# Performance work log

Measured on AMD Instinct MI355X. Metric: run time of the kernel, lower is better.

Reference implementation:

```python
import jax, jax.numpy as jnp
import numpy as np

H, HD, RD = 16, 128, 64          # n_heads, head_dim, rope_dim
CD = HD - RD                      # content_dim = 64
THETA = 10000.0


def apply_rope(x, cos, sin):
    # x: [B,H,T,RD]; cos/sin: [T,RD//2] broadcast over B,H
    d = x.shape[-1] // 2
    x1, x2 = x[..., :d], x[..., d:]
    return jnp.concatenate([x1 * cos - x2 * sin, x1 * sin + x2 * cos], axis=-1)


def setup_inputs() -> dict:
    key = jax.random.key(0)
    ks = jax.random.split(key, 9)
    d_model, q_rank, d_latent = 2048, 512, 512
    B, T = 2, 2048
    s = 0.02
    return {
        "x": jax.random.normal(ks[0], (B, T, d_model), dtype=jnp.float32),
        "Wq_down": jax.random.normal(ks[1], (d_model, q_rank), dtype=jnp.float32) * s,
        "Wq_up": jax.random.normal(ks[2], (q_rank, H * CD), dtype=jnp.float32) * s,
        "Wq_rope": jax.random.normal(ks[3], (d_model, H * RD), dtype=jnp.float32) * s,
        "Wkv_down": jax.random.normal(ks[4], (d_model, d_latent), dtype=jnp.float32) * s,
        "Wk_up": jax.random.normal(ks[5], (d_latent, H * CD), dtype=jnp.float32) * s,
        "Wv_up": jax.random.normal(ks[6], (d_latent, H * HD), dtype=jnp.float32) * s,
        "Wk_rope": jax.random.normal(ks[7], (d_model, H * RD), dtype=jnp.float32) * s,
        "Wo": jax.random.normal(ks[8], (H * HD, d_model), dtype=jnp.float32) * s,
    }


def reference(x, Wq_down, Wq_up, Wq_rope, Wkv_down, Wk_up, Wv_up, Wk_rope, Wo):
    B, T, _ = x.shape

    # low-rank projections
    q_content = (x @ Wq_down) @ Wq_up            # [B,T,H*CD]
    q_pos = x @ Wq_rope                          # [B,T,H*RD]
    kv_latent = x @ Wkv_down                     # [B,T,d_latent]
    k_content = kv_latent @ Wk_up                # [B,T,H*CD]
    k_pos = x @ Wk_rope                          # [B,T,H*RD]
    v = kv_latent @ Wv_up                        # [B,T,H*HD]

    def split_heads(t, d):
        return t.reshape(B, T, H, d).transpose(0, 2, 1, 3)  # [B,H,T,d]

    q_content = split_heads(q_content, CD)
    q_pos = split_heads(q_pos, RD)
    k_content = split_heads(k_content, CD)
    k_pos = split_heads(k_pos, RD)
    v = split_heads(v, HD)

    # rotary tables: [T, RD//2]
    inv_freq = 1.0 / (THETA ** (jnp.arange(0, RD, 2, dtype=jnp.float32) / RD))
    freqs = jnp.arange(T, dtype=jnp.float32)[:, None] * inv_freq[None, :]
    cos, sin = jnp.cos(freqs), jnp.sin(freqs)

    q_pos = apply_rope(q_pos, cos, sin)
    k_pos = apply_rope(k_pos, cos, sin)

    q = jnp.concatenate([q_content, q_pos], axis=-1)  # [B,H,T,HD]
    k = jnp.concatenate([k_content, k_pos], axis=-1)  # [B,H,T,HD]

    # causal SDPA, scale = 1/sqrt(head_dim)
    scale = 1.0 / jnp.sqrt(jnp.asarray(HD, dtype=q.dtype))
    scores = jnp.einsum("bhqd,bhkd->bhqk", q, k) * scale
    causal = jnp.tril(jnp.ones((T, T), dtype=bool))
    scores = jnp.where(causal, scores, jnp.finfo(scores.dtype).min)
    attn = jax.nn.softmax(scores, axis=-1)
    out = jnp.einsum("bhqk,bhkd->bhqd", attn, v)      # [B,H,T,HD]

    out = out.transpose(0, 2, 1, 3).reshape(B, T, H * HD)
    return out @ Wo
```

## Files before the change

### kernel.cpp

```cpp
#include <hip/hip_runtime.h>
#include <hip/hip_bf16.h>
#include <stdint.h>
#include <math.h>

#define H_ 16
#define HD_ 128
#define RD_ 64
#define CD_ 64
#define DM_ 2048
#define QR_ 512
#define DL_ 512
#define B_ 2
#define T_ 2048
#define M_TOT (B_*T_)

typedef __attribute__((ext_vector_type(8))) short short8;
typedef __attribute__((ext_vector_type(4))) float f32x4;
typedef __attribute__((ext_vector_type(16))) float f32x16;

__device__ __forceinline__ unsigned short f2b_hw(float f){
  __hip_bfloat16 h = __float2bfloat16(f);
  union { __hip_bfloat16 h; unsigned short u; } c; c.h = h; return c.u;
}
__device__ __forceinline__ float b2f(unsigned short b){
  union { unsigned u; float f; } a; a.u = ((unsigned)b) << 16;
  return a.f;
}
__device__ __forceinline__ unsigned pack2(float lo, float hi){
  __hip_bfloat162 h2 = __float22bfloat162_rn(make_float2(lo, hi));
  union { __hip_bfloat162 h; unsigned u; } c; c.h = h2; return c.u;
}

#define GLOAD16(g, l) __builtin_amdgcn_global_load_lds( \
    (__attribute__((address_space(1))) void*)(g), \
    (__attribute__((address_space(3))) void*)(l), 16, 0, 0)

__global__ void cast_f32_bf16(const float* __restrict__ src,
                              unsigned short* __restrict__ dst, int n){
  int i = (blockIdx.x * blockDim.x + threadIdx.x) * 4;
  if (i < n){
    float4 v = *(const float4*)(src + i);
    ushort4 o;
    o.x = f2b_hw(v.x); o.y = f2b_hw(v.y); o.z = f2b_hw(v.z); o.w = f2b_hw(v.w);
    *(ushort4*)(dst + i) = o;
  }
}

__global__ void rope_table(float2* __restrict__ tab){
  int idx = blockIdx.x * 256 + threadIdx.x;
  int t = idx >> 5, j = idx & 31;
  float invf = exp2f(-(float)j * 0.4152410118750f);
  float fr = (float)t * invf;
  float s, c;
  sincosf(fr, &s, &c);
  tab[idx] = make_float2(c, s);
}

struct TTe { const float* src; unsigned short* dst; int K, N, blk0; };
struct TT8 { TTe e[8]; };

__global__ void transpose_cast8(TT8 tab){
  __shared__ float tile[32][33];
  int bid = blockIdx.x;
  const float* src = tab.e[0].src;
  unsigned short* dst = tab.e[0].dst;
  int K = tab.e[0].K, N = tab.e[0].N, loc = bid;
  #pragma unroll
  for (int j = 1; j < 8; j++){
    if (bid >= tab.e[j].blk0){
      src = tab.e[j].src; dst = tab.e[j].dst;
      K = tab.e[j].K; N = tab.e[j].N; loc = bid - tab.e[j].blk0;
    }
  }
  int cols = N / 32;
  int n0 = (loc % cols) * 32, k0 = (loc / cols) * 32;
  int tx = threadIdx.x, ty = threadIdx.y;
  #pragma unroll
  for (int r = ty; r < 32; r += 8)
    tile[r][tx] = src[(size_t)(k0 + r) * N + n0 + tx];
  __syncthreads();
  #pragma unroll
  for (int r = ty; r < 32; r += 8)
    dst[(size_t)(n0 + r) * K + k0 + tx] = f2b_hw(tile[tx][r]);
}

template<int MODE>
__global__ __launch_bounds__(512, 1) void gemm256(
    const unsigned short* __restrict__ A, int lda,
    const unsigned short* __restrict__ Bt,
    void* __restrict__ Cv, void* __restrict__ Cv2, void* __restrict__ Cv3,
    const float2* __restrict__ tab,
    int ldc, int N, int K)
{
  __shared__ __align__(16) unsigned short lds[65536];
  char* ldsb = (char*)lds;

  const int tid = threadIdx.x;
  const int lane = tid & 63, w = tid >> 6;
  const int wm = w >> 2, wn = w & 3;
  const int l15 = lane & 15, kg = lane >> 4;

  int gx = gridDim.x;
  int nwg = gx * gridDim.y;
  int lin = blockIdx.x + gx * blockIdx.y;
  int q8 = nwg >> 3;
  int nl = (lin & 7) * q8 + (lin >> 3);
  int m0 = (nl / gx) * 256, n0 = (nl % gx) * 256;

  const unsigned short* Aeff = A;
  if (MODE == 5 && n0 >= 1024) Aeff = A + 512;

  const int srow = tid >> 3;
  const int scol = ((((tid & 7) << 4) ^ (((tid >> 5) & 1) << 5)) >> 1);
  const int aswz = ((l15 >> 2) & 1) << 5;

#define STG(bufb, kt) do {                                                     \
    int k0_ = (kt) * 64;                                                       \
    _Pragma("unroll")                                                          \
    for (int h_ = 0; h_ < 2; h_++)                                             \
      _Pragma("unroll")                                                        \
      for (int i_ = 0; i_ < 2; i_++) {                                         \
        GLOAD16(Aeff + (size_t)(m0 + h_*128 + i_*64 + srow) * lda + k0_ + scol,\
                ldsb + (bufb)*65536 + h_*16384 + i_*8192 + tid*16);            \
        GLOAD16(Bt + (size_t)(n0 + h_*128 + i_*64 + srow) * K + k0_ + scol,    \
                ldsb + (bufb)*65536 + 32768 + h_*16384 + i_*8192 + tid*16);    \
      }                                                                        \
  } while (0)

  f32x4 acc[8][4];
  #pragma unroll
  for (int i = 0; i < 8; i++)
    #pragma unroll
    for (int j = 0; j < 4; j++)
      acc[i][j] = (f32x4){0.f, 0.f, 0.f, 0.f};

  const int nK = K >> 6;
  STG(0, 0);
  STG(1, 1);

  for (int t = 0; t < nK; t++) {
    const int c = t & 1;
    if (t < nK - 1) { asm volatile("s_waitcnt vmcnt(8)" ::: "memory"); }
    else            { asm volatile("s_waitcnt vmcnt(0)" ::: "memory"); }
    __builtin_amdgcn_s_barrier();
    __builtin_amdgcn_sched_barrier(0);

    const char* bufA = ldsb + c * 65536 + wm * 16384;
    const char* bufB = ldsb + c * 65536 + 32768;

    short8 bfr[4][2];
    #pragma unroll
    for (int nf = 0; nf < 4; nf++) {
      int nr = wn * 64 + nf * 16 + l15;
      #pragma unroll
      for (int kk = 0; kk < 2; kk++) {
        int L = (nr & 127) * 128 + kk * 64 + kg * 16;
        bfr[nf][kk] = *(const short8*)(bufB + (nr >> 7) * 16384 + (L ^ aswz));
      }
    }
    __builtin_amdgcn_s_setprio(1);
    #pragma unroll
    for (int mh = 0; mh < 2; mh++) {
      short8 afr[4][2];
      #pragma unroll
      for (int q = 0; q < 4; q++) {
        int mf = mh * 4 + q;
        #pragma unroll
        for (int kk = 0; kk < 2; kk++) {
          int L = (mf * 16 + l15) * 128 + kk * 64 + kg * 16;
          afr[q][kk] = *(const short8*)(bufA + (L ^ aswz));
        }
      }
      #pragma unroll
      for (int q = 0; q < 4; q++)
        #pragma unroll
        for (int nf = 0; nf < 4; nf++)
          #pragma unroll
          for (int kk = 0; kk < 2; kk++)
            acc[mh*4+q][nf] = __builtin_amdgcn_mfma_f32_16x16x32_bf16(
                afr[q][kk], bfr[nf][kk], acc[mh*4+q][nf], 0, 0, 0);
    }
    __builtin_amdgcn_s_setprio(0);
    __builtin_amdgcn_sched_barrier(0);
    __builtin_amdgcn_s_barrier();
    __builtin_amdgcn_sched_barrier(0);
    if (t + 2 < nK) STG(c, t + 2);
  }
#undef STG

  if (MODE == 4) {
    if (n0 < 1024) {
      unsigned short* C = (unsigned short*)Cv;
      #pragma unroll
      for (int mf = 0; mf < 8; mf++)
        #pragma unroll
        for (int nf = 0; nf < 4; nf++)
          #pragma unroll
          for (int rr = 0; rr < 4; rr++) {
            int row = m0 + wm * 128 + mf * 16 + kg * 4 + rr;
            int col = n0 + wn * 64 + nf * 16 + l15;
            C[(size_t)row * ldc + col] = f2b_hw(acc[mf][nf][rr]);
          }
    } else {
      const bool isq = (n0 < 2048);
      unsigned short* dst = (unsigned short*)(isq ? Cv2 : Cv3);
      int hbase = ((n0 - (isq ? 1024 : 2048)) >> 6) + wn;
      #pragma unroll
      for (int nf = 0; nf < 2; nf++) {
        int jr = nf * 16 + l15;
        #pragma unroll
        for (int mf = 0; mf < 8; mf++)
          #pragma unroll
          for (int rr = 0; rr < 4; rr++) {
            int gr = m0 + wm * 128 + mf * 16 + kg * 4 + rr;
            int tt = gr & (T_ - 1), bb = gr >> 11;
            float2 cs = tab[tt * 32 + jr];
            float x1 = acc[mf][nf][rr], x2 = acc[mf][nf + 2][rr];
            size_t base = ((size_t)(bb * H_ + hbase) * T_ + tt) * 128 + 64;
            dst[base + jr]      = f2b_hw(x1 * cs.x - x2 * cs.y);
            dst[base + jr + 32] = f2b_hw(x1 * cs.y + x2 * cs.x);
          }
      }
    }
  } else {
    if (n0 < 2048) {
      unsigned short* dstp = (unsigned short*)(n0 < 1024 ? Cv : Cv2);
      int cb0 = n0 - (n0 < 1024 ? 0 : 1024);
      #pragma unroll
      for (int nf = 0; nf < 4; nf++) {
        int colb = cb0 + wn * 64 + nf * 16 + l15;
        int h = colb >> 6, d = colb & 63;
        #pragma unroll
        for (int mf = 0; mf < 8; mf++)
          #pragma unroll
          for (int rr = 0; rr < 4; rr++) {
            int gr = m0 + wm * 128 + mf * 16 + kg * 4 + rr;
            size_t idx = ((size_t)((gr >> 11) * H_ + h) * T_ + (gr & (T_-1))) * 128 + d;
            dstp[idx] = f2b_hw(acc[mf][nf][rr]);
          }
      }
    } else {
      unsigned short* vtp = (unsigned short*)Cv3;
      #pragma unroll
      for (int nf = 0; nf < 4; nf++) {
        int c2 = n0 + wn * 64 + nf * 16 + l15 - 2048;
        int h = c2 >> 7, d = c2 & 127;
        #pragma unroll
        for (int mf = 0; mf < 8; mf++) {
          int gr0 = m0 + wm * 128 + mf * 16 + kg * 4;
          int bb = gr0 >> 11, t0 = gr0 & (T_-1);
          ushort4 o;
          o.x = f2b_hw(acc[mf][nf][0]); o.y = f2b_hw(acc[mf][nf][1]);
          o.z = f2b_hw(acc[mf][nf][2]); o.w = f2b_hw(acc[mf][nf][3]);
          *(ushort4*)&vtp[((size_t)(bb * H_ + h) * 128 + d) * T_ + t0] = o;
        }
      }
    }
  }
}

__global__ __launch_bounds__(512, 1) void gemm_out(
    const unsigned short* __restrict__ A, int lda,
    const unsigned short* __restrict__ Bt,
    float* __restrict__ C, int ldc, int K)
{
  __shared__ __align__(16) unsigned short lds[49152];
  char* ldsb = (char*)lds;

  const int tid = threadIdx.x;
  const int lane = tid & 63, w = tid >> 6;
  const int wm = w >> 2, wn = w & 3;
  const int l15 = lane & 15, kg = lane >> 4;

  int gx = gridDim.x;
  int nwg = gx * gridDim.y;
  int lin = blockIdx.x + gx * blockIdx.y;
  int q8 = nwg >> 3;
  int nl = (lin & 7) * q8 + (lin >> 3);
  int m0 = (nl / gx) * 128, n0 = (nl % gx) * 256;

  const int srow = tid >> 3;
  const int scol = ((((tid & 7) << 4) ^ (((tid >> 5) & 1) << 5)) >> 1);
  const int aswz = ((l15 >> 2) & 1) << 5;

#define STG(bufb, kt) do {                                                     \
    int k0_ = (kt) * 64;                                                       \
    _Pragma("unroll")                                                          \
    for (int i_ = 0; i_ < 2; i_++)                                             \
      GLOAD16(A + (size_t)(m0 + i_*64 + srow) * lda + k0_ + scol,              \
              ldsb + (bufb)*49152 + i_*8192 + tid*16);                         \
    _Pragma("unroll")                                                          \
    for (int i_ = 0; i_ < 4; i_++)                                             \
      GLOAD16(Bt + (size_t)(n0 + i_*64 + srow) * K + k0_ + scol,               \
              ldsb + (bufb)*49152 + 16384 + i_*8192 + tid*16);                 \
  } while (0)

  f32x4 acc[4][4];
  #pragma unroll
  for (int i = 0; i < 4; i++)
    #pragma unroll
    for (int j = 0; j < 4; j++)
      acc[i][j] = (f32x4){0.f, 0.f, 0.f, 0.f};

  const int nK = K >> 6;
  STG(0, 0);
  STG(1, 1);

  for (int t = 0; t < nK; t++) {
    const int c = t & 1;
    if (t < nK - 1) { asm volatile("s_waitcnt vmcnt(6)" ::: "memory"); }
    else            { asm volatile("s_waitcnt vmcnt(0)" ::: "memory"); }
    __builtin_amdgcn_s_barrier();
    __builtin_amdgcn_sched_barrier(0);

    const char* bufA = ldsb + c * 49152 + wm * 8192;
    const char* bufB = ldsb + c * 49152 + 16384;

    short8 bfr[4][2];
    #pragma unroll
    for (int nf = 0; nf < 4; nf++) {
      int nr = wn * 64 + nf * 16 + l15;
      #pragma unroll
      for (int kk = 0; kk < 2; kk++) {
        int L = (nr & 63) * 128 + kk * 64 + kg * 16;
        bfr[nf][kk] = *(const short8*)(bufB + (nr >> 6) * 8192 + (L ^ aswz));
      }
    }
    short8 afr[4][2];
    #pragma unroll
    for (int mf = 0; mf < 4; mf++)
      #pragma unroll
      for (int kk = 0; kk < 2; kk++) {
        int L = (mf * 16 + l15) * 128 + kk * 64 + kg * 16;
        afr[mf][kk] = *(const short8*)(bufA + (L ^ aswz));
      }
    __builtin_amdgcn_s_setprio(1);
    #pragma unroll
    for (int mf = 0; mf < 4; mf++)
      #pragma unroll
      for (int nf = 0; nf < 4; nf++)
        #pragma unroll
        for (int kk = 0; kk < 2; kk++)
          acc[mf][nf] = __builtin_amdgcn_mfma_f32_16x16x32_bf16(
              afr[mf][kk], bfr[nf][kk], acc[mf][nf], 0, 0, 0);
    __builtin_amdgcn_s_setprio(0);
    __builtin_amdgcn_sched_barrier(0);
    __builtin_amdgcn_s_barrier();
    __builtin_amdgcn_sched_barrier(0);
    if (t + 2 < nK) STG(c, t + 2);
  }
#undef STG

  #pragma unroll
  for (int mf = 0; mf < 4; mf++)
    #pragma unroll
    for (int nf = 0; nf < 4; nf++)
      #pragma unroll
      for (int rr = 0; rr < 4; rr++) {
        int row = m0 + wm * 64 + mf * 16 + kg * 4 + rr;
        int col = n0 + wn * 64 + nf * 16 + l15;
        C[(size_t)row * ldc + col] = acc[mf][nf][rr];
      }
}

__global__ __launch_bounds__(256, 2) void attn_fwd7(
    const unsigned short* __restrict__ qh,
    const unsigned short* __restrict__ kh,
    const unsigned short* __restrict__ vt,
    unsigned short* __restrict__ ao)
{
  __shared__ __align__(16) unsigned short lds[4 * 8192];

  const int tid  = threadIdx.x;
  const int lane = tid & 63, w = tid >> 6;
  const int l31  = lane & 31, hi = lane >> 5;
  const int bh = blockIdx.y;
  const int b  = bh >> 4, hd = bh & 15;
  int qt = blockIdx.x;
  if (bh >= 16) qt = 15 - qt;
  const int q0w   = qt * 128 + w * 32;
  const int qg    = q0w + l31;
  const int qmaxw = q0w + 31;
  const int nt    = 2 * qt + 2;

  const unsigned short* Qg = qh + (size_t)bh * T_ * 128;
  const unsigned short* Kg = kh + (size_t)bh * T_ * 128;
  const unsigned short* Vg = vt + (size_t)bh * 128 * T_;

  short8 qf[8];
  #pragma unroll
  for (int kc = 0; kc < 8; kc++)
    qf[kc] = *(const short8*)&Qg[(size_t)qg * 128 + kc * 16 + hi * 8];

  f32x16 accO[4];
  #pragma unroll
  for (int sb = 0; sb < 4; sb++)
    #pragma unroll
    for (int r = 0; r < 16; r++) accO[sb][r] = 0.f;

  float m = -1e30f, lsum = 0.f;
  const float SC = 0.12751743f;

  int krow[4], kwof[4], vrow[4], vwof[4];
  #pragma unroll
  for (int jj = 0; jj < 4; jj++){
    int r_ = (w * 4 + jj) * 4 + (lane >> 4);
    krow[jj] = r_;
    kwof[jj] = r_ * 128 + ((((lane & 15) * 16) ^ ((r_ & 7) << 4)) >> 1);
    int d_ = (w * 4 + jj) * 8 + (lane >> 3);
    vrow[jj] = d_;
    vwof[jj] = d_ * 64 + ((((lane & 7) * 16) ^ ((d_ & 7) << 4)) >> 1);
  }
  const int kcol = (lane & 15) * 8;
  const int vcol = (lane & 7) * 8;

  uint4 kst[4], vst[4];

#define REG_LOAD(kvt) do {                                                    \
    int kv0s = (kvt) * 64;                                                    \
    _Pragma("unroll")                                                         \
    for (int j_ = 0; j_ < 4; j_++) {                                          \
      kst[j_] = *(const uint4*)&Kg[(size_t)(kv0s + krow[j_]) * 128 + kcol];   \
      vst[j_] = *(const uint4*)&Vg[(size_t)vrow[j_] * T_ + kv0s + vcol];      \
    }                                                                         \
  } while (0)

#define DS_WRITE(bufi) do {                                                   \
    unsigned short* ksb_ = lds + (bufi) * 8192;                               \
    unsigned short* vsb_ = lds + 16384 + (bufi) * 8192;                       \
    _Pragma("unroll")                                                         \
    for (int j_ = 0; j_ < 4; j_++) {                                          \
      *(uint4*)&ksb_[kwof[j_]] = kst[j_];                                     \
      *(uint4*)&vsb_[vwof[j_]] = vst[j_];                                     \
    }                                                                         \
  } while (0)

  REG_LOAD(0);
  DS_WRITE(0);
  if (nt > 1) REG_LOAD(1);
  asm volatile("s_waitcnt lgkmcnt(0)" ::: "memory");
  __builtin_amdgcn_s_barrier();
  __builtin_amdgcn_sched_barrier(0);

  for (int t = 0; t < nt; t++) {
    const int cur = t & 1;
    if (t + 1 < nt) DS_WRITE(cur ^ 1);
    if (t + 2 < nt) REG_LOAD(t + 2);
    const int kv0 = t * 64;
    if (kv0 <= qmaxw) {
      const unsigned short* Kb = lds + cur * 8192;
      const unsigned short* Vb = lds + 16384 + cur * 8192;

      f32x16 sa0, sa1;
      #pragma unroll
      for (int r = 0; r < 16; r++) { sa0[r] = 0.f; sa1[r] = 0.f; }
      __builtin_amdgcn_s_setprio(1);
      #pragma unroll
      for (int kc = 0; kc < 8; kc++) {
        int co = (kc * 32 + hi * 16);
        int r0 = l31;
        short8 kf0 = *(const short8*)&Kb[r0 * 128 + ((co ^ ((r0 & 7) << 4)) >> 1)];
        sa0 = __builtin_amdgcn_mfma_f32_32x32x16_bf16(kf0, qf[kc], sa0, 0, 0, 0);
        int r1 = 32 + l31;
        short8 kf1 = *(const short8*)&Kb[r1 * 128 + ((co ^ ((r1 & 7) << 4)) >> 1)];
        sa1 = __builtin_amdgcn_mfma_f32_32x32x16_bf16(kf1, qf[kc], sa1, 0, 0, 0);
      }
      __builtin_amdgcn_s_setprio(0);

      float p0[16], p1[16];
      float pmax = -1e30f;
      bool needMask = (kv0 + 63 > q0w);
      if (needMask) {
        #pragma unroll
        for (int r = 0; r < 16; r++) {
          int crow = (r & 3) + 8 * (r >> 2) + 4 * hi;
          float v0 = sa0[r] * SC;
          float v1 = sa1[r] * SC;
          if (kv0 + crow > qg)      v0 = -1e30f;
          if (kv0 + 32 + crow > qg) v1 = -1e30f;
          p0[r] = v0; p1[r] = v1;
          pmax = fmaxf(pmax, fmaxf(v0, v1));
        }
      } else {
        #pragma unroll
        for (int r = 0; r < 16; r++) {
          float v0 = sa0[r] * SC;
          float v1 = sa1[r] * SC;
          p0[r] = v0; p1[r] = v1;
          pmax = fmaxf(pmax, fmaxf(v0, v1));
        }
      }
      pmax = fmaxf(pmax, __shfl_xor(pmax, 32, 64));
      if (!__all(pmax <= m + 8.f)) {
        float mn  = fmaxf(m, pmax);
        float fac = exp2f(m - mn);
        m = mn;
        lsum *= fac;
        #pragma unroll
        for (int sb = 0; sb < 4; sb++)
          #pragma unroll
          for (int r = 0; r < 16; r++) accO[sb][r] *= fac;
      }
      float ls = 0.f;
      #pragma unroll
      for (int r = 0; r < 16; r++) {
        p0[r] = exp2f(p0[r] - m);
        p1[r] = exp2f(p1[r] - m);
        ls += p0[r] + p1[r];
      }
      ls += __shfl_xor(ls, 32, 64);
      lsum += ls;

      #pragma unroll
      for (int kc2 = 0; kc2 < 4; kc2++) {
        unsigned A01, A23, B01, B23;
        if (kc2 == 0) { A01 = pack2(p0[0], p0[1]);  A23 = pack2(p0[2], p0[3]);
                        B01 = pack2(p0[4], p0[5]);  B23 = pack2(p0[6], p0[7]); }
        else if (kc2 == 1) { A01 = pack2(p0[8], p0[9]);   A23 = pack2(p0[10], p0[11]);
                             B01 = pack2(p0[12], p0[13]); B23 = pack2(p0[14], p0[15]); }
        else if (kc2 == 2) { A01 = pack2(p1[0], p1[1]);  A23 = pack2(p1[2], p1[3]);
                             B01 = pack2(p1[4], p1[5]);  B23 = pack2(p1[6], p1[7]); }
        else { A01 = pack2(p1[8], p1[9]);   A23 = pack2(p1[10], p1[11]);
               B01 = pack2(p1[12], p1[13]); B23 = pack2(p1[14], p1[15]); }
        asm("v_permlane32_swap_b32 %0, %1" : "+v"(A01), "+v"(B01));
        asm("v_permlane32_swap_b32 %0, %1" : "+v"(A23), "+v"(B23));
        union { unsigned u[4]; short8 v; } pk;
        pk.u[0] = A01; pk.u[1] = A23; pk.u[2] = B01; pk.u[3] = B23;
        short8 pa = pk.v;
        __builtin_amdgcn_s_setprio(1);
        #pragma unroll
        for (int sb = 0; sb < 4; sb++) {
          int d = sb * 32 + l31;
          short8 vf = *(const short8*)&Vb[d * 64 + (((kc2 * 32 + hi * 16) ^ ((d & 7) << 4)) >> 1)];
          accO[sb] = __builtin_amdgcn_mfma_f32_32x32x16_bf16(vf, pa, accO[sb], 0, 0, 0);
        }
        __builtin_amdgcn_s_setprio(0);
      }
    }
    __builtin_amdgcn_sched_barrier(0);
    asm volatile("s_waitcnt lgkmcnt(0)" ::: "memory");
    __builtin_amdgcn_s_barrier();
    __builtin_amdgcn_sched_barrier(0);
  }

  float rl = 1.0f / lsum;
  size_t orow = ((size_t)b * T_ + qg) * (H_*HD_) + hd * 128;
  #pragma unroll
  for (int sb = 0; sb < 4; sb++)
    #pragma unroll
    for (int g = 0; g < 4; g++) {
      ushort4 o;
      o.x = f2b_hw(accO[sb][4 * g + 0] * rl);
      o.y = f2b_hw(accO[sb][4 * g + 1] * rl);
      o.z = f2b_hw(accO[sb][4 * g + 2] * rl);
      o.w = f2b_hw(accO[sb][4 * g + 3] * rl);
      *(ushort4*)&ao[orow + sb * 32 + 8 * g + 4 * hi] = o;
    }
#undef REG_LOAD
#undef DS_WRITE
}

extern "C" void kernel_launch(void* const* d_in, const int* in_sizes, int n_in,
                              void* d_out, int out_size, void* d_ws, size_t ws_size,
                              hipStream_t stream)
{
  (void)in_sizes; (void)n_in; (void)out_size; (void)ws_size;
  const float* x        = (const float*)d_in[0];
  const float* Wq_down  = (const float*)d_in[1];
  const float* Wq_up    = (const float*)d_in[2];
  const float* Wq_rope  = (const float*)d_in[3];
  const float* Wkv_down = (const float*)d_in[4];
  const float* Wk_up    = (const float*)d_in[5];
  const float* Wv_up    = (const float*)d_in[6];
  const float* Wk_rope  = (const float*)d_in[7];
  const float* Wo       = (const float*)d_in[8];

  char* ws = (char*)d_ws;
  unsigned short* xb      = (unsigned short*)(ws + 0);
  unsigned short* Wdall   = (unsigned short*)(ws + 16777216);
  unsigned short* WquT    = (unsigned short*)(ws + 29360128);
  unsigned short* WkcvT   = (unsigned short*)(ws + 30408704);
  unsigned short* WoT     = (unsigned short*)(ws + 33554432);
  unsigned short* projall = (unsigned short*)(ws + 41943040);
  unsigned short* qh      = (unsigned short*)(ws + 67108864);
  unsigned short* kh      = (unsigned short*)(ws + 83886080);
  unsigned short* vt      = (unsigned short*)(ws + 100663296);
  unsigned short* ao      = (unsigned short*)(ws + 117440512);
  float2*         ctab    = (float2*)(ws + 134217728);

  dim3 tb(32, 8);

  cast_f32_bf16<<<(M_TOT * DM_ / 4 + 255) / 256, 256, 0, stream>>>(x, xb, M_TOT * DM_);
  rope_table<<<256, 256, 0, stream>>>(ctab);

  TT8 tab;
  int blk = 0;
  tab.e[0] = { Wq_down,  Wdall,               DM_, QR_,     blk }; blk += (QR_/32)*(DM_/32);
  tab.e[1] = { Wkv_down, Wdall + 512*2048,    DM_, DL_,     blk }; blk += (DL_/32)*(DM_/32);
  tab.e[2] = { Wq_rope,  Wdall + 1024*2048,   DM_, H_*RD_,  blk }; blk += (H_*RD_/32)*(DM_/32);
  tab.e[3] = { Wk_rope,  Wdall + 2048*2048,   DM_, H_*RD_,  blk }; blk += (H_*RD_/32)*(DM_/32);
  tab.e[4] = { Wq_up,    WquT,                QR_, H_*CD_,  blk }; blk += (H_*CD_/32)*(QR_/32);
  tab.e[5] = { Wk_up,    WkcvT,               DL_, H_*CD_,  blk }; blk += (H_*CD_/32)*(DL_/32);
  tab.e[6] = { Wv_up,    WkcvT + 1024*512,    DL_, H_*HD_,  blk }; blk += (H_*HD_/32)*(DL_/32);
  tab.e[7] = { Wo,       WoT,                 H_*HD_, DM_,  blk }; blk += (DM_/32)*(H_*HD_/32);
  transpose_cast8<<<blk, tb, 0, stream>>>(tab);

  gemm256<4><<<dim3(3072/256, M_TOT/256), 512, 0, stream>>>(
      xb, DM_, Wdall, projall, qh, kh, ctab, 1024, 3072, DM_);
  gemm256<5><<<dim3(4096/256, M_TOT/256), 512, 0, stream>>>(
      projall, 1024, WquT, qh, kh, vt, nullptr, 0, 4096, DL_);

  attn_fwd7<<<dim3(16, 32), 256, 0, stream>>>(qh, kh, vt, ao);

  gemm_out<<<dim3(DM_/256, M_TOT/128), 512, 0, stream>>>(
      ao, 2048, WoT, (float*)d_out, DM_, H_*HD_);
}
```

Measured before the change: 301.4 us.

## Merge rope table into cast kernel, vectorize weight transpose, split QK accumulators

Folds the rope cos/sin table generation into the x cast kernel as extra blocks, which saves one kernel launch. The weight transpose-cast now uses float4 loads and ushort4 stores with an 8x32 thread block. In the attention kernel, the QK^T MFMA chain is split into two independent accumulator pairs that are summed at the end. This shortens MFMA dependency chains at the cost of more accumulator registers, which may put pressure on occupancy. The LDS pattern in the transpose changes and may introduce bank conflicts.

```diff
diff --git a/kernel.cpp b/kernel.cpp
--- a/kernel.cpp
+++ b/kernel.cpp
@@ -36,24 +36,26 @@
     (__attribute__((address_space(3))) void*)(l), 16, 0, 0)
 
 __global__ void cast_f32_bf16(const float* __restrict__ src,
-                              unsigned short* __restrict__ dst, int n){
-  int i = (blockIdx.x * blockDim.x + threadIdx.x) * 4;
+                              unsigned short* __restrict__ dst, int n,
+                              float2* __restrict__ tab){
+  int bid = blockIdx.x;
+  if (bid >= 8192) {
+    int idx = (bid - 8192) * 256 + threadIdx.x;
+    int t = idx >> 5, j = idx & 31;
+    float invf = exp2f(-(float)j * 0.4152410118750f);
+    float fr = (float)t * invf;
+    float s, c;
+    sincosf(fr, &s, &c);
+    tab[idx] = make_float2(c, s);
+    return;
+  }
+  int i = (bid * 256 + threadIdx.x) * 4;
   if (i < n){
     float4 v = *(const float4*)(src + i);
     ushort4 o;
     o.x = f2b_hw(v.x); o.y = f2b_hw(v.y); o.z = f2b_hw(v.z); o.w = f2b_hw(v.w);
     *(ushort4*)(dst + i) = o;
   }
-}
-
-__global__ void rope_table(float2* __restrict__ tab){
-  int idx = blockIdx.x * 256 + threadIdx.x;
-  int t = idx >> 5, j = idx & 31;
-  float invf = exp2f(-(float)j * 0.4152410118750f);
-  float fr = (float)t * invf;
-  float s, c;
-  sincosf(fr, &s, &c);
-  tab[idx] = make_float2(c, s);
 }
 
 struct TTe { const float* src; unsigned short* dst; int K, N, blk0; };
@@ -75,13 +77,18 @@
   int cols = N / 32;
   int n0 = (loc % cols) * 32, k0 = (loc / cols) * 32;
   int tx = threadIdx.x, ty = threadIdx.y;
-  #pragma unroll
-  for (int r = ty; r < 32; r += 8)
-    tile[r][tx] = src[(size_t)(k0 + r) * N + n0 + tx];
+  float4 v = *(const float4*)&src[(size_t)(k0 + ty) * N + n0 + tx * 4];
+  tile[ty][tx * 4 + 0] = v.x;
+  tile[ty][tx * 4 + 1] = v.y;
+  tile[ty][tx * 4 + 2] = v.z;
+  tile[ty][tx * 4 + 3] = v.w;
   __syncthreads();
-  #pragma unroll
-  for (int r = ty; r < 32; r += 8)
-    dst[(size_t)(n0 + r) * K + k0 + tx] = f2b_hw(tile[tx][r]);
+  ushort4 o;
+  o.x = f2b_hw(tile[tx * 4 + 0][ty]);
+  o.y = f2b_hw(tile[tx * 4 + 1][ty]);
+  o.z = f2b_hw(tile[tx * 4 + 2][ty]);
+  o.w = f2b_hw(tile[tx * 4 + 3][ty]);
+  *(ushort4*)&dst[(size_t)(n0 + ty) * K + k0 + tx * 4] = o;
 }
 
 template<int MODE>
@@ -363,7 +370,7 @@
       }
 }
 
-__global__ __launch_bounds__(256, 2) void attn_fwd7(
+__global__ __launch_bounds__(256, 2) void attn_fwd8(
     const unsigned short* __restrict__ qh,
     const unsigned short* __restrict__ kh,
     const unsigned short* __restrict__ vt,
@@ -451,21 +458,27 @@
       const unsigned short* Kb = lds + cur * 8192;
       const unsigned short* Vb = lds + 16384 + cur * 8192;
 
-      f32x16 sa0, sa1;
-      #pragma unroll
-      for (int r = 0; r < 16; r++) { sa0[r] = 0.f; sa1[r] = 0.f; }
+      f32x16 sa0, sa1, sb0, sb1;
+      #pragma unroll
+      for (int r = 0; r < 16; r++) { sa0[r] = 0.f; sa1[r] = 0.f; sb0[r] = 0.f; sb1[r] = 0.f; }
       __builtin_amdgcn_s_setprio(1);
       #pragma unroll
-      for (int kc = 0; kc < 8; kc++) {
-        int co = (kc * 32 + hi * 16);
-        int r0 = l31;
-        short8 kf0 = *(const short8*)&Kb[r0 * 128 + ((co ^ ((r0 & 7) << 4)) >> 1)];
-        sa0 = __builtin_amdgcn_mfma_f32_32x32x16_bf16(kf0, qf[kc], sa0, 0, 0, 0);
-        int r1 = 32 + l31;
-        short8 kf1 = *(const short8*)&Kb[r1 * 128 + ((co ^ ((r1 & 7) << 4)) >> 1)];
-        sa1 = __builtin_amdgcn_mfma_f32_32x32x16_bf16(kf1, qf[kc], sa1, 0, 0, 0);
+      for (int kc = 0; kc < 8; kc += 2) {
+        int co0 = (kc * 32 + hi * 16);
+        int co1 = ((kc + 1) * 32 + hi * 16);
+        int r0 = l31, r1 = 32 + l31;
+        short8 kf0a = *(const short8*)&Kb[r0 * 128 + ((co0 ^ ((r0 & 7) << 4)) >> 1)];
+        short8 kf1a = *(const short8*)&Kb[r1 * 128 + ((co0 ^ ((r1 & 7) << 4)) >> 1)];
+        short8 kf0b = *(const short8*)&Kb[r0 * 128 + ((co1 ^ ((r0 & 7) << 4)) >> 1)];
+        short8 kf1b = *(const short8*)&Kb[r1 * 128 + ((co1 ^ ((r1 & 7) << 4)) >> 1)];
+        sa0 = __builtin_amdgcn_mfma_f32_32x32x16_bf16(kf0a, qf[kc], sa0, 0, 0, 0);
+        sa1 = __builtin_amdgcn_mfma_f32_32x32x16_bf16(kf1a, qf[kc], sa1, 0, 0, 0);
+        sb0 = __builtin_amdgcn_mfma_f32_32x32x16_bf16(kf0b, qf[kc + 1], sb0, 0, 0, 0);
+        sb1 = __builtin_amdgcn_mfma_f32_32x32x16_bf16(kf1b, qf[kc + 1], sb1, 0, 0, 0);
       }
       __builtin_amdgcn_s_setprio(0);
+      sa0 += sb0;
+      sa1 += sb1;
 
       float p0[16], p1[16];
       float pmax = -1e30f;
@@ -588,10 +601,7 @@
   unsigned short* ao      = (unsigned short*)(ws + 117440512);
   float2*         ctab    = (float2*)(ws + 134217728);
 
-  dim3 tb(32, 8);
-
-  cast_f32_bf16<<<(M_TOT * DM_ / 4 + 255) / 256, 256, 0, stream>>>(x, xb, M_TOT * DM_);
-  rope_table<<<256, 256, 0, stream>>>(ctab);
+  cast_f32_bf16<<<8192 + 256, 256, 0, stream>>>(x, xb, M_TOT * DM_, ctab);
 
   TT8 tab;
   int blk = 0;
@@ -603,14 +613,14 @@
   tab.e[5] = { Wk_up,    WkcvT,               DL_, H_*CD_,  blk }; blk += (H_*CD_/32)*(DL_/32);
   tab.e[6] = { Wv_up,    WkcvT + 1024*512,    DL_, H_*HD_,  blk }; blk += (H_*HD_/32)*(DL_/32);
   tab.e[7] = { Wo,       WoT,                 H_*HD_, DM_,  blk }; blk += (DM_/32)*(H_*HD_/32);
-  transpose_cast8<<<blk, tb, 0, stream>>>(tab);
+  transpose_cast8<<<blk, dim3(8, 32), 0, stream>>>(tab);
 
   gemm256<4><<<dim3(3072/256, M_TOT/256), 512, 0, stream>>>(
       xb, DM_, Wdall, projall, qh, kh, ctab, 1024, 3072, DM_);
   gemm256<5><<<dim3(4096/256, M_TOT/256), 512, 0, stream>>>(
       projall, 1024, WquT, qh, kh, vt, nullptr, 0, 4096, DL_);
 
-  attn_fwd7<<<dim3(16, 32), 256, 0, stream>>>(qh, kh, vt, ao);
+  attn_fwd8<<<dim3(16, 32), 256, 0, stream>>>(qh, kh, vt, ao);
 
   gemm_out<<<dim3(DM_/256, M_TOT/128), 512, 0, stream>>>(
       ao, 2048, WoT, (float*)d_out, DM_, H_*HD_);
```

After: 292.4 us (median of 2 runs). -3.0%, faster.
